# Kernel tuning notes

Hardware: AMD Instinct MI355X
Metric: run time of the kernel (lower is better)

## Reference

```python
import jax, jax.numpy as jnp
import numpy as np

H = 128
NUM_IN = 384
B, N, K = 4, 2048, 48
SCALE = 30.0
EPS = 1e-5


def _layernorm(x, gamma, beta):
    mu = jnp.mean(x, axis=-1, keepdims=True)
    var = jnp.mean(jnp.square(x - mu), axis=-1, keepdims=True)
    return (x - mu) * jax.lax.rsqrt(var + EPS) * gamma + beta


def setup_inputs() -> dict:
    key = jax.random.key(0)
    ks = jax.random.split(key, 12)
    s = lambda fan_in: 1.0 / np.sqrt(fan_in)
    inp = {
        "h_V": jax.random.normal(ks[0], (B, N, H), jnp.float32),
        "h_E": jax.random.normal(ks[1], (B, N, K, NUM_IN), jnp.float32),
        "mask_V": jnp.ones((B, N), jnp.float32),
        "mask_attend": jnp.ones((B, N, K), jnp.float32),
        # message MLP
        "W1": jax.random.uniform(ks[2], (H + NUM_IN, H), jnp.float32, -s(H + NUM_IN), s(H + NUM_IN)),
        "b1": jnp.zeros((H,), jnp.float32),
        "W2": jax.random.uniform(ks[3], (H, H), jnp.float32, -s(H), s(H)),
        "b2": jnp.zeros((H,), jnp.float32),
        "W3": jax.random.uniform(ks[4], (H, H), jnp.float32, -s(H), s(H)),
        "b3": jnp.zeros((H,), jnp.float32),
        # layernorms
        "g1": jnp.ones((H,), jnp.float32), "be1": jnp.zeros((H,), jnp.float32),
        "g2": jnp.ones((H,), jnp.float32), "be2": jnp.zeros((H,), jnp.float32),
        # FFN
        "Wi": jax.random.uniform(ks[5], (H, 4 * H), jnp.float32, -s(H), s(H)),
        "bi": jnp.zeros((4 * H,), jnp.float32),
        "Wo": jax.random.uniform(ks[6], (4 * H, H), jnp.float32, -s(4 * H), s(4 * H)),
        "bo": jnp.zeros((H,), jnp.float32),
        # rezero alpha (init 0.01)
        "alpha": jnp.array([0.01], jnp.float32),
    }
    return inp


def reference(h_V, h_E, mask_V, mask_attend, W1, b1, W2, b2, W3, b3,
              g1, be1, g2, be2, Wi, bi, Wo, bo, alpha):
    gelu = lambda x: jax.nn.gelu(x, approximate=False)
    # broadcast-concat node features onto each neighbor edge: [B,N,K,H+num_in]
    h_V_expand = jnp.broadcast_to(h_V[:, :, None, :], (*h_E.shape[:-1], h_V.shape[-1]))
    h_EV = jnp.concatenate([h_V_expand, h_E], axis=-1)
    # 3-layer message MLP
    h_message = gelu(jnp.einsum("bnkf,fh->bnkh", h_EV, W1) + b1)
    h_message = gelu(jnp.einsum("bnkh,hg->bnkg", h_message, W2) + b2)
    h_message = jnp.einsum("bnkg,gh->bnkh", h_message, W3) + b3
    h_message = mask_attend[..., None] * h_message
    # masked sum-reduce over neighbors
    dh = jnp.sum(h_message, axis=-2) / SCALE
    # residual (rezero) + LayerNorm  (dropout = identity in eval)
    h = _layernorm(alpha * dh + h_V, g1, be1)
    # position-wise FFN
    dh = gelu(h @ Wi + bi) @ Wo + bo
    h = _layernorm(alpha * dh + h, g2, be2)
    # node mask
    h = mask_V[..., None] * h
    return h
```

## Files before the change

### kernel.cpp

```cpp
#include <hip/hip_runtime.h>

#define LN_EPS 1e-5f
#define RSCALE (1.0f / 30.0f)

typedef short short8  __attribute__((ext_vector_type(8)));
typedef short short4v __attribute__((ext_vector_type(4)));
typedef float f32x4   __attribute__((ext_vector_type(4)));

__device__ __forceinline__ unsigned short f2bf(float f) {
    unsigned u = __builtin_bit_cast(unsigned, f);
    u = u + 0x7FFFu + ((u >> 16) & 1u);
    return (unsigned short)(u >> 16);
}

__device__ __forceinline__ float gelu_f(float x) {
    float u  = 0.7978845608028654f * (x + 0.044715f * x * x * x);
    float e  = __expf(-2.0f * fabsf(u));
    float t  = 1.0f - 2.0f * e / (1.0f + e);
    return 0.5f * x * (1.0f + copysignf(t, u));
}

__device__ __forceinline__ f32x4 zero4() {
    f32x4 v; v.x = 0.f; v.y = 0.f; v.z = 0.f; v.w = 0.f; return v;
}

__global__ __launch_bounds__(256) void prep_w(
    const float* __restrict__ W1, const float* __restrict__ W2,
    const float* __restrict__ W3,
    unsigned short* __restrict__ w1bt, unsigned short* __restrict__ w2t,
    unsigned short* __restrict__ w3t)
{
    int t = blockIdx.x * 256 + threadIdx.x;
    if (t < 49152) {
        int m = t & 127, kk = t >> 7;
        w1bt[m * 384 + kk] = f2bf(W1[(kk + 128) * 128 + m]);
    } else if (t < 65536) {
        int u = t - 49152, m = u & 127, k = u >> 7;
        w2t[m * 128 + k] = f2bf(W2[k * 128 + m]);
    } else if (t < 81920) {
        int u = t - 65536, m = u & 127, k = u >> 7;
        w3t[m * 128 + k] = f2bf(W3[k * 128 + m]);
    }
}

__global__ __launch_bounds__(256, 3) void edge_mlp(
    const float* __restrict__ hV, const float* __restrict__ hE,
    const float* __restrict__ mAtt,
    const float* __restrict__ W1, const float* __restrict__ b1,
    const unsigned short* __restrict__ w1bt, const unsigned short* __restrict__ w2t,
    const unsigned short* __restrict__ w3t,
    const float* __restrict__ b2, const float* __restrict__ b3,
    float* __restrict__ dh)
{
    __shared__ __align__(16) short A1[96 * 64];
    __shared__ __align__(16) short Wb[128 * 64];
    __shared__ __align__(16) short Hb[96 * 128];
    __shared__ float mb[96];

    const int tid  = threadIdx.x;
    const int lane = tid & 63;
    const int wv   = tid >> 6;
    const int g    = wv & 1;
    const int mh   = wv >> 1;
    const int ln   = lane & 15;
    const int kg   = lane >> 4;
    const int node0 = blockIdx.x * 2;

    const int srow = tid >> 4;
    const int c4   = (tid & 15) * 4;
    const int kb_w = c4 >> 3;
    const int c4lo = c4 & 4;

    if (tid < 96) mb[tid] = mAtt[node0 * 48 + tid];

    float* nv = (float*)A1;
    {
        const int gg = tid >> 7, m = tid & 127;
        const float* hv = hV + (node0 + gg) * 128;
        const float* wc = W1 + m;
        float a0 = 0.f, a1 = 0.f, a2 = 0.f, a3 = 0.f;
        for (int k = 0; k < 128; k += 4) {
            const float4 h4 = *(const float4*)(hv + k);
            a0 += h4.x * wc[(k + 0) * 128];
            a1 += h4.y * wc[(k + 1) * 128];
            a2 += h4.z * wc[(k + 2) * 128];
            a3 += h4.w * wc[(k + 3) * 128];
        }
        nv[tid] = b1[m] + (a0 + a1) + (a2 + a3);
    }
    __syncthreads();

    f32x4 acc[4][3];
#pragma unroll
    for (int j = 0; j < 4; ++j) {
        const float4 iv = *(const float4*)&nv[g * 128 + (4 * mh + j) * 16 + kg * 4];
#pragma unroll
        for (int i = 0; i < 3; ++i) {
            acc[j][i].x = iv.x; acc[j][i].y = iv.y;
            acc[j][i].z = iv.z; acc[j][i].w = iv.w;
        }
    }
    __syncthreads();

    for (int c = 0; c < 6; ++c) {
        const int kc = c * 64;
#pragma unroll
        for (int rep = 0; rep < 6; ++rep) {
            const int r = rep * 16 + srow;
            const float4 v = *(const float4*)(hE + (node0 * 48 + r) * 384 + kc + c4);
            short4v p;
            p.x = (short)f2bf(v.x); p.y = (short)f2bf(v.y);
            p.z = (short)f2bf(v.z); p.w = (short)f2bf(v.w);
            *(short4v*)&A1[r * 64 + ((kb_w ^ (r & 7)) * 8) + c4lo] = p;
        }
#pragma unroll
        for (int rep = 0; rep < 4; ++rep) {
            const int u = rep * 256 + tid;
            const int m = u >> 3, kb = u & 7;
            short8 val = *(const short8*)(w1bt + m * 384 + kc + kb * 8);
            *(short8*)&Wb[m * 64 + ((kb ^ (m & 7)) * 8)] = val;
        }
        __syncthreads();
#pragma unroll
        for (int s = 0; s < 2; ++s) {
            const int kb = s * 4 + kg;
            short8 bf[3], af[4];
#pragma unroll
            for (int i = 0; i < 3; ++i) {
                const int r = (3 * g + i) * 16 + ln;
                bf[i] = *(const short8*)&A1[r * 64 + ((kb ^ (r & 7)) * 8)];
            }
#pragma unroll
            for (int j = 0; j < 4; ++j) {
                const int m = (4 * mh + j) * 16 + ln;
                af[j] = *(const short8*)&Wb[m * 64 + ((kb ^ (m & 7)) * 8)];
            }
#pragma unroll
            for (int j = 0; j < 4; ++j)
#pragma unroll
                for (int i = 0; i < 3; ++i)
                    acc[j][i] = __builtin_amdgcn_mfma_f32_16x16x32_bf16(af[j], bf[i], acc[j][i], 0, 0, 0);
        }
        __syncthreads();
    }

#pragma unroll
    for (int j = 0; j < 4; ++j) {
        const int m0 = (4 * mh + j) * 16 + kg * 4;
#pragma unroll
        for (int i = 0; i < 3; ++i) {
            const int r = (3 * g + i) * 16 + ln;
            short4v p;
            p.x = (short)f2bf(gelu_f(acc[j][i].x));
            p.y = (short)f2bf(gelu_f(acc[j][i].y));
            p.z = (short)f2bf(gelu_f(acc[j][i].z));
            p.w = (short)f2bf(gelu_f(acc[j][i].w));
            *(short4v*)&Hb[r * 128 + (((m0 >> 3) ^ (r & 7)) * 8) + (m0 & 4)] = p;
        }
    }

    for (int L = 0; L < 2; ++L) {
#pragma unroll
        for (int j = 0; j < 4; ++j)
#pragma unroll
            for (int i = 0; i < 3; ++i) acc[j][i] = zero4();

        const unsigned short* wt = (L == 0) ? w2t : w3t;
        for (int c = 0; c < 2; ++c) {
            const int kc = c * 64;
#pragma unroll
            for (int rep = 0; rep < 4; ++rep) {
                const int u = rep * 256 + tid;
                const int m = u >> 3, kb = u & 7;
                short8 val = *(const short8*)(wt + m * 128 + kc + kb * 8);
                *(short8*)&Wb[m * 64 + ((kb ^ (m & 7)) * 8)] = val;
            }
            __syncthreads();
#pragma unroll
            for (int s = 0; s < 2; ++s) {
                const int kbW = s * 4 + kg;
                const int kbH = c * 8 + s * 4 + kg;
                short8 bf[3], af[4];
#pragma unroll
                for (int i = 0; i < 3; ++i) {
                    const int r = (3 * g + i) * 16 + ln;
                    bf[i] = *(const short8*)&Hb[r * 128 + ((kbH ^ (r & 7)) * 8)];
                }
#pragma unroll
                for (int j = 0; j < 4; ++j) {
                    const int m = (4 * mh + j) * 16 + ln;
                    af[j] = *(const short8*)&Wb[m * 64 + ((kbW ^ (m & 7)) * 8)];
                }
#pragma unroll
                for (int j = 0; j < 4; ++j)
#pragma unroll
                    for (int i = 0; i < 3; ++i)
                        acc[j][i] = __builtin_amdgcn_mfma_f32_16x16x32_bf16(af[j], bf[i], acc[j][i], 0, 0, 0);
            }
            __syncthreads();
        }

        if (L == 0) {
#pragma unroll
            for (int j = 0; j < 4; ++j) {
                const int m0 = (4 * mh + j) * 16 + kg * 4;
                const float4 bb = *(const float4*)(b2 + m0);
#pragma unroll
                for (int i = 0; i < 3; ++i) {
                    const int r = (3 * g + i) * 16 + ln;
                    short4v p;
                    p.x = (short)f2bf(gelu_f(acc[j][i].x + bb.x));
                    p.y = (short)f2bf(gelu_f(acc[j][i].y + bb.y));
                    p.z = (short)f2bf(gelu_f(acc[j][i].z + bb.z));
                    p.w = (short)f2bf(gelu_f(acc[j][i].w + bb.w));
                    *(short4v*)&Hb[r * 128 + (((m0 >> 3) ^ (r & 7)) * 8) + (m0 & 4)] = p;
                }
            }
        } else {
#pragma unroll
            for (int j = 0; j < 4; ++j) {
                const int m0 = (4 * mh + j) * 16 + kg * 4;
                const float4 bb = *(const float4*)(b3 + m0);
                float s0 = 0.f, s1 = 0.f, s2 = 0.f, s3 = 0.f;
#pragma unroll
                for (int i = 0; i < 3; ++i) {
                    const int r = (3 * g + i) * 16 + ln;
                    const float mk = mb[r];
                    s0 += (acc[j][i].x + bb.x) * mk;
                    s1 += (acc[j][i].y + bb.y) * mk;
                    s2 += (acc[j][i].z + bb.z) * mk;
                    s3 += (acc[j][i].w + bb.w) * mk;
                }
#pragma unroll
                for (int off = 1; off < 16; off <<= 1) {
                    s0 += __shfl_xor(s0, off, 64);
                    s1 += __shfl_xor(s1, off, 64);
                    s2 += __shfl_xor(s2, off, 64);
                    s3 += __shfl_xor(s3, off, 64);
                }
                if (ln == 0) {
                    float4 o;
                    o.x = s0 * RSCALE; o.y = s1 * RSCALE;
                    o.z = s2 * RSCALE; o.w = s3 * RSCALE;
                    *(float4*)&dh[(node0 + g) * 128 + m0] = o;
                }
            }
        }
    }
}

__global__ __launch_bounds__(256, 2) void node_ffn(
    const float* __restrict__ hV, const float* __restrict__ dh,
    const float* __restrict__ maskV,
    const float* __restrict__ g1, const float* __restrict__ be1,
    const float* __restrict__ g2, const float* __restrict__ be2,
    const float* __restrict__ Wi, const float* __restrict__ bi,
    const float* __restrict__ Wo, const float* __restrict__ bo,
    const float* __restrict__ alphap, float* __restrict__ out)
{
    __shared__ float hbuf[16 * 132];
    __shared__ float hidb[16 * 516];
    __shared__ float obuf[16 * 132];

    const int tid = threadIdx.x;
    const float al = alphap[0];
    const int nb = blockIdx.x * 16;

    {
        const int m = tid >> 4, s = tid & 15;
        const int i0 = s * 8;
        const int base = (nb + m) * 128 + i0;
        float x[8];
        {
            float4 a0 = *(const float4*)(dh + base);
            float4 a1 = *(const float4*)(dh + base + 4);
            float4 v0 = *(const float4*)(hV + base);
            float4 v1 = *(const float4*)(hV + base + 4);
            x[0] = v0.x + al * a0.x; x[1] = v0.y + al * a0.y;
            x[2] = v0.z + al * a0.z; x[3] = v0.w + al * a0.w;
            x[4] = v1.x + al * a1.x; x[5] = v1.y + al * a1.y;
            x[6] = v1.z + al * a1.z; x[7] = v1.w + al * a1.w;
        }
        float sm = 0.f;
#pragma unroll
        for (int q = 0; q < 8; ++q) sm += x[q];
#pragma unroll
        for (int off = 1; off < 16; off <<= 1) sm += __shfl_xor(sm, off, 64);
        const float mu = sm * (1.0f / 128.0f);
        float vs = 0.f;
#pragma unroll
        for (int q = 0; q < 8; ++q) { float d = x[q] - mu; vs += d * d; }
#pragma unroll
        for (int off = 1; off < 16; off <<= 1) vs += __shfl_xor(vs, off, 64);
        const float rs = rsqrtf(vs * (1.0f / 128.0f) + LN_EPS);
#pragma unroll
        for (int q = 0; q < 8; ++q)
            hbuf[m * 132 + i0 + q] = (x[q] - mu) * rs * g1[i0 + q] + be1[i0 + q];
    }
    __syncthreads();

    {
        const int jg = tid & 127, mhh = tid >> 7;
        const int j4 = jg * 4;
        float acc[8][4];
#pragma unroll
        for (int mm = 0; mm < 8; ++mm)
#pragma unroll
            for (int jj = 0; jj < 4; ++jj) acc[mm][jj] = 0.f;
        for (int i0 = 0; i0 < 128; i0 += 4) {
            float4 w0 = *(const float4*)(Wi + (i0 + 0) * 512 + j4);
            float4 w1 = *(const float4*)(Wi + (i0 + 1) * 512 + j4);
            float4 w2 = *(const float4*)(Wi + (i0 + 2) * 512 + j4);
            float4 w3 = *(const float4*)(Wi + (i0 + 3) * 512 + j4);
#pragma unroll
            for (int mm = 0; mm < 8; ++mm) {
                float4 h4 = *(const float4*)&hbuf[(mhh * 8 + mm) * 132 + i0];
                acc[mm][0] += h4.x * w0.x + h4.y * w1.x + h4.z * w2.x + h4.w * w3.x;
                acc[mm][1] += h4.x * w0.y + h4.y * w1.y + h4.z * w2.y + h4.w * w3.y;
                acc[mm][2] += h4.x * w0.z + h4.y * w1.z + h4.z * w2.z + h4.w * w3.z;
                acc[mm][3] += h4.x * w0.w + h4.y * w1.w + h4.z * w2.w + h4.w * w3.w;
            }
        }
        float4 bb = *(const float4*)(bi + j4);
#pragma unroll
        for (int mm = 0; mm < 8; ++mm) {
            float4 o;
            o.x = gelu_f(acc[mm][0] + bb.x);
            o.y = gelu_f(acc[mm][1] + bb.y);
            o.z = gelu_f(acc[mm][2] + bb.z);
            o.w = gelu_f(acc[mm][3] + bb.w);
            *(float4*)&hidb[(mhh * 8 + mm) * 516 + j4] = o;
        }
    }
    __syncthreads();

    {
        const int m = tid >> 4;
        const int n8 = (tid & 15) * 8;
        float4 r0, r1;
        r0.x = r0.y = r0.z = r0.w = 0.f;
        r1.x = r1.y = r1.z = r1.w = 0.f;
        for (int j0 = 0; j0 < 512; j0 += 4) {
            float4 hh = *(const float4*)&hidb[m * 516 + j0];
            float hq[4] = {hh.x, hh.y, hh.z, hh.w};
#pragma unroll
            for (int jj = 0; jj < 4; ++jj) {
                float4 w0 = *(const float4*)(Wo + (j0 + jj) * 128 + n8);
                float4 w1 = *(const float4*)(Wo + (j0 + jj) * 128 + n8 + 4);
                r0.x += hq[jj] * w0.x; r0.y += hq[jj] * w0.y;
                r0.z += hq[jj] * w0.z; r0.w += hq[jj] * w0.w;
                r1.x += hq[jj] * w1.x; r1.y += hq[jj] * w1.y;
                r1.z += hq[jj] * w1.z; r1.w += hq[jj] * w1.w;
            }
        }
        float4 q0 = *(const float4*)(bo + n8);
        float4 q1 = *(const float4*)(bo + n8 + 4);
        r0.x += q0.x; r0.y += q0.y; r0.z += q0.z; r0.w += q0.w;
        r1.x += q1.x; r1.y += q1.y; r1.z += q1.z; r1.w += q1.w;
        *(float4*)&obuf[m * 132 + n8]     = r0;
        *(float4*)&obuf[m * 132 + n8 + 4] = r1;
    }
    __syncthreads();

    {
        const int m = tid >> 4, s = tid & 15;
        const int i0 = s * 8;
        float x[8];
#pragma unroll
        for (int q = 0; q < 8; ++q)
            x[q] = hbuf[m * 132 + i0 + q] + al * obuf[m * 132 + i0 + q];
        float sm = 0.f;
#pragma unroll
        for (int q = 0; q < 8; ++q) sm += x[q];
#pragma unroll
        for (int off = 1; off < 16; off <<= 1) sm += __shfl_xor(sm, off, 64);
        const float mu = sm * (1.0f / 128.0f);
        float vs = 0.f;
#pragma unroll
        for (int q = 0; q < 8; ++q) { float d = x[q] - mu; vs += d * d; }
#pragma unroll
        for (int off = 1; off < 16; off <<= 1) vs += __shfl_xor(vs, off, 64);
        const float rs = rsqrtf(vs * (1.0f / 128.0f) + LN_EPS);
        const float mk = maskV[nb + m];
        float y[8];
#pragma unroll
        for (int q = 0; q < 8; ++q)
            y[q] = ((x[q] - mu) * rs * g2[i0 + q] + be2[i0 + q]) * mk;
        float4 o0, o1;
        o0.x = y[0]; o0.y = y[1]; o0.z = y[2]; o0.w = y[3];
        o1.x = y[4]; o1.y = y[5]; o1.z = y[6]; o1.w = y[7];
        const int base = (nb + m) * 128 + i0;
        *(float4*)(out + base)     = o0;
        *(float4*)(out + base + 4) = o1;
    }
}

extern "C" void kernel_launch(void* const* d_in, const int* in_sizes, int n_in,
                              void* d_out, int out_size, void* d_ws, size_t ws_size,
                              hipStream_t stream)
{
    const float* hV  = (const float*)d_in[0];
    const float* hE  = (const float*)d_in[1];
    const float* mV  = (const float*)d_in[2];
    const float* mA  = (const float*)d_in[3];
    const float* W1  = (const float*)d_in[4];
    const float* b1  = (const float*)d_in[5];
    const float* W2  = (const float*)d_in[6];
    const float* b2  = (const float*)d_in[7];
    const float* W3  = (const float*)d_in[8];
    const float* b3  = (const float*)d_in[9];
    const float* g1  = (const float*)d_in[10];
    const float* be1 = (const float*)d_in[11];
    const float* g2  = (const float*)d_in[12];
    const float* be2 = (const float*)d_in[13];
    const float* Wi  = (const float*)d_in[14];
    const float* bi  = (const float*)d_in[15];
    const float* Wo  = (const float*)d_in[16];
    const float* bo  = (const float*)d_in[17];
    const float* al  = (const float*)d_in[18];
    float* out = (float*)d_out;

    float* dh = (float*)d_ws;
    unsigned short* w1bt = (unsigned short*)((char*)d_ws + (size_t)4194304);
    unsigned short* w2t = w1bt + 49152;
    unsigned short* w3t = w2t + 16384;

    prep_w  <<<320,  256, 0, stream>>>(W1, W2, W3, w1bt, w2t, w3t);
    edge_mlp<<<4096, 256, 0, stream>>>(hV, hE, mA, W1, b1, w1bt, w2t, w3t, b2, b3, dh);
    node_ffn<<<512,  256, 0, stream>>>(hV, dh, mV, g1, be1, g2, be2, Wi, bi, Wo, bo, al, out);
}
```

Before: 938.7 us.

## Prefetch h_E chunks into registers and use transposed bf16 W1 for node projection

The edge MLP now loads the next 64-column h_E chunk into registers while the MFMA work on the current chunk runs, so global load latency overlaps with compute. The first h_E chunk is issued before the per-node projection, which now reads h_V from shared memory and a bf16 transposed copy of the top part of W1 made in prep_w, with contiguous 16-byte loads instead of strided fp32 loads. This adds 24 float registers per thread under a 3-blocks-per-SM launch bound, which may cause spills or lower occupancy. The node projection also drops to bf16 weight precision.

```diff
diff --git a/kernel.cpp b/kernel.cpp
--- a/kernel.cpp
+++ b/kernel.cpp
@@ -11,6 +11,10 @@
     unsigned u = __builtin_bit_cast(unsigned, f);
     u = u + 0x7FFFu + ((u >> 16) & 1u);
     return (unsigned short)(u >> 16);
+}
+
+__device__ __forceinline__ float bf2f(unsigned short h) {
+    return __builtin_bit_cast(float, (unsigned)h << 16);
 }
 
 __device__ __forceinline__ float gelu_f(float x) {
@@ -28,7 +32,7 @@
     const float* __restrict__ W1, const float* __restrict__ W2,
     const float* __restrict__ W3,
     unsigned short* __restrict__ w1bt, unsigned short* __restrict__ w2t,
-    unsigned short* __restrict__ w3t)
+    unsigned short* __restrict__ w3t, unsigned short* __restrict__ w1at)
 {
     int t = blockIdx.x * 256 + threadIdx.x;
     if (t < 49152) {
@@ -40,15 +44,18 @@
     } else if (t < 81920) {
         int u = t - 65536, m = u & 127, k = u >> 7;
         w3t[m * 128 + k] = f2bf(W3[k * 128 + m]);
+    } else if (t < 98304) {
+        int u = t - 81920, m = u & 127, k = u >> 7;
+        w1at[m * 128 + k] = f2bf(W1[k * 128 + m]);
     }
 }
 
 __global__ __launch_bounds__(256, 3) void edge_mlp(
     const float* __restrict__ hV, const float* __restrict__ hE,
     const float* __restrict__ mAtt,
-    const float* __restrict__ W1, const float* __restrict__ b1,
+    const float* __restrict__ b1,
     const unsigned short* __restrict__ w1bt, const unsigned short* __restrict__ w2t,
-    const unsigned short* __restrict__ w3t,
+    const unsigned short* __restrict__ w3t, const unsigned short* __restrict__ w1at,
     const float* __restrict__ b2, const float* __restrict__ b3,
     float* __restrict__ dh)
 {
@@ -73,20 +80,37 @@
 
     if (tid < 96) mb[tid] = mAtt[node0 * 48 + tid];
 
+    float4 pv[6];
+#pragma unroll
+    for (int rep = 0; rep < 6; ++rep)
+        pv[rep] = *(const float4*)(hE + (node0 * 48 + rep * 16 + srow) * 384 + c4);
+
+    {
+        float* hvs = (float*)A1 + 256;
+        hvs[tid] = hV[(node0 + (tid >> 7)) * 128 + (tid & 127)];
+    }
+    __syncthreads();
+
     float* nv = (float*)A1;
     {
         const int gg = tid >> 7, m = tid & 127;
-        const float* hv = hV + (node0 + gg) * 128;
-        const float* wc = W1 + m;
+        const float* hv = (const float*)A1 + 256 + gg * 128;
+        const unsigned short* wa = w1at + m * 128;
         float a0 = 0.f, a1 = 0.f, a2 = 0.f, a3 = 0.f;
-        for (int k = 0; k < 128; k += 4) {
-            const float4 h4 = *(const float4*)(hv + k);
-            a0 += h4.x * wc[(k + 0) * 128];
-            a1 += h4.y * wc[(k + 1) * 128];
-            a2 += h4.z * wc[(k + 2) * 128];
-            a3 += h4.w * wc[(k + 3) * 128];
-        }
-        nv[tid] = b1[m] + (a0 + a1) + (a2 + a3);
+        for (int k = 0; k < 128; k += 8) {
+            short8 w8 = *(const short8*)(wa + k);
+            a0 += hv[k + 0] * bf2f((unsigned short)w8[0]);
+            a1 += hv[k + 1] * bf2f((unsigned short)w8[1]);
+            a2 += hv[k + 2] * bf2f((unsigned short)w8[2]);
+            a3 += hv[k + 3] * bf2f((unsigned short)w8[3]);
+            a0 += hv[k + 4] * bf2f((unsigned short)w8[4]);
+            a1 += hv[k + 5] * bf2f((unsigned short)w8[5]);
+            a2 += hv[k + 6] * bf2f((unsigned short)w8[6]);
+            a3 += hv[k + 7] * bf2f((unsigned short)w8[7]);
+        }
+        const float r = b1[m] + (a0 + a1) + (a2 + a3);
+        __syncthreads();
+        nv[tid] = r;
     }
     __syncthreads();
 
@@ -107,10 +131,9 @@
 #pragma unroll
         for (int rep = 0; rep < 6; ++rep) {
             const int r = rep * 16 + srow;
-            const float4 v = *(const float4*)(hE + (node0 * 48 + r) * 384 + kc + c4);
             short4v p;
-            p.x = (short)f2bf(v.x); p.y = (short)f2bf(v.y);
-            p.z = (short)f2bf(v.z); p.w = (short)f2bf(v.w);
+            p.x = (short)f2bf(pv[rep].x); p.y = (short)f2bf(pv[rep].y);
+            p.z = (short)f2bf(pv[rep].z); p.w = (short)f2bf(pv[rep].w);
             *(short4v*)&A1[r * 64 + ((kb_w ^ (r & 7)) * 8) + c4lo] = p;
         }
 #pragma unroll
@@ -121,6 +144,13 @@
             *(short8*)&Wb[m * 64 + ((kb ^ (m & 7)) * 8)] = val;
         }
         __syncthreads();
+        if (c < 5) {
+#pragma unroll
+            for (int rep = 0; rep < 6; ++rep) {
+                const int r = rep * 16 + srow;
+                pv[rep] = *(const float4*)(hE + (node0 * 48 + r) * 384 + (kc + 64) + c4);
+            }
+        }
 #pragma unroll
         for (int s = 0; s < 2; ++s) {
             const int kb = s * 4 + kg;
@@ -422,10 +452,11 @@
 
     float* dh = (float*)d_ws;
     unsigned short* w1bt = (unsigned short*)((char*)d_ws + (size_t)4194304);
-    unsigned short* w2t = w1bt + 49152;
-    unsigned short* w3t = w2t + 16384;
-
-    prep_w  <<<320,  256, 0, stream>>>(W1, W2, W3, w1bt, w2t, w3t);
-    edge_mlp<<<4096, 256, 0, stream>>>(hV, hE, mA, W1, b1, w1bt, w2t, w3t, b2, b3, dh);
+    unsigned short* w2t  = w1bt + 49152;
+    unsigned short* w3t  = w2t + 16384;
+    unsigned short* w1at = w3t + 16384;
+
+    prep_w  <<<384,  256, 0, stream>>>(W1, W2, W3, w1bt, w2t, w3t, w1at);
+    edge_mlp<<<4096, 256, 0, stream>>>(hV, hE, mA, b1, w1bt, w2t, w3t, w1at, b2, b3, dh);
     node_ffn<<<512,  256, 0, stream>>>(hV, dh, mV, g1, be1, g2, be2, Wi, bi, Wo, bo, al, out);
 }
```

After: 932.6 us. About the same (-0.6%).
